# Optimization experiments

Measured on AMD Instinct MI355X. Metric: run time of the kernel, lower is better.

The kernel has to match this reference:

```python
import jax, jax.numpy as jnp
import numpy as np
from jax import lax

Q = 4          # decimation factor
N_ORDER = 8    # IIR filter order (scipy decimate default / explicit n=8)
RP = 0.05      # passband ripple in dB used by scipy.signal.decimate


def _cheby1_ba(N, rp, Wn):
    """Chebyshev type-I lowpass design, identical math to scipy.signal.cheby1."""
    eps = np.sqrt(10.0 ** (0.1 * rp) - 1.0)
    mu = np.arcsinh(1.0 / eps) / N
    k = np.arange(1, N + 1)
    theta = np.pi * (2 * k - 1) / (2 * N)
    # analog prototype poles (cheb1ap)
    p = -np.sinh(mu) * np.sin(theta) + 1j * np.cosh(mu) * np.cos(theta)
    g = np.prod(-p).real
    if N % 2 == 0:
        g /= np.sqrt(1.0 + eps ** 2)
    # frequency pre-warp (iirfilter with fs=2.0)
    fs = 2.0
    warped = 2.0 * fs * np.tan(np.pi * Wn / fs)
    # lp2lp_zpk
    p = p * warped
    g = g * warped ** N
    # bilinear_zpk
    fs2 = 2.0 * fs
    pd = (fs2 + p) / (fs2 - p)
    zd = -np.ones(N)  # N zeros at z=-1
    gd = g * np.real(1.0 / np.prod(fs2 - p))
    b = np.real(gd * np.poly(zd))
    a = np.real(np.poly(pd))
    return b, a


def _lfilter_zi(b, a):
    """Steady-state initial conditions, identical math to scipy.signal.lfilter_zi."""
    n = len(a)
    comp = np.zeros((n - 1, n - 1))
    comp[0, :] = -a[1:] / a[0]
    comp[1:, :-1] = np.eye(n - 2)
    IminusA = np.eye(n - 1) - comp.T
    B = b[1:] - a[1:] * b[0]
    return np.linalg.solve(IminusA, B)


_B_NP, _A_NP = _cheby1_ba(N_ORDER, RP, 0.8 / Q)
_ZI_NP = _lfilter_zi(_B_NP, _A_NP)


def _lfilter(b, a, x, zi):
    """IIR filter, direct-form II transposed. x: (T, M), zi: (order, M)."""
    def step(z, xt):
        yt = b[0] * xt + z[0]                       # (M,)
        z = jnp.concatenate([z[1:], jnp.zeros_like(z[:1])], axis=0) \
            + b[1:, None] * xt[None, :] - a[1:, None] * yt[None, :]
        return z, yt
    _, y = lax.scan(step, zi, x)
    return y


def _filtfilt(b, a, zi, x):
    """scipy.signal.filtfilt with padtype='odd', padlen=3*max(len(a),len(b)). x: (T, M)."""
    edge = 3 * b.shape[0]  # 27 for an order-8 filter
    left = 2.0 * x[0] - x[edge:0:-1]            # odd extension, left
    right = 2.0 * x[-1] - x[-2:-(edge + 2):-1]  # odd extension, right
    ext = jnp.concatenate([left, x, right], axis=0)
    y = _lfilter(b, a, ext, zi[:, None] * ext[0][None, :])          # forward pass
    y = _lfilter(b, a, y[::-1], zi[:, None] * y[-1][None, :])[::-1]  # backward pass
    return y[edge:-edge]


def _decimate(x):
    """scipy.signal.decimate(x, q=Q, n=8, ftype='iir', axis=-1, zero_phase=True)."""
    B_, C_, T = x.shape
    b = jnp.asarray(_B_NP, x.dtype)
    a = jnp.asarray(_A_NP, x.dtype)
    zi = jnp.asarray(_ZI_NP, x.dtype)
    xt = x.reshape(B_ * C_, T).T  # (T, M) -- time leading for lax.scan
    y = _filtfilt(b, a, zi, xt)
    y = y.T.reshape(B_, C_, T)
    return y[..., ::Q]


def setup_inputs() -> dict:
    key = jax.random.key(0)
    x = jax.random.normal(key, (32, 16, 65536), dtype=jnp.float32)
    return {"x": x}


def reference(x):
    return _decimate(x)
```

## Files before the change

kernel.cpp:

```cpp
#include <hip/hip_runtime.h>
#include <cmath>
#include <complex>

namespace {

constexpr int TLEN   = 65536;
constexpr int NCH    = 512;
constexpr size_t YB_ROWS = 16400;


struct Coefs {
  float b0,b1,b2,b3,b4,b5,b6,b7,b8;
  float na1,na2,na3,na4,na5,na6,na7,na8;
  float zi0,zi1,zi2,zi3,zi4,zi5,zi6,zi7;
};

#define IIR_STEP(xv, yv)                                  \
  do {                                                    \
    yv = fmaf(cf.b0, (xv), z0);                           \
    z0 = fmaf(cf.na1, yv, fmaf(cf.b1, (xv), z1));         \
    z1 = fmaf(cf.na2, yv, fmaf(cf.b2, (xv), z2));         \
    z2 = fmaf(cf.na3, yv, fmaf(cf.b3, (xv), z3));         \
    z3 = fmaf(cf.na4, yv, fmaf(cf.b4, (xv), z4));         \
    z4 = fmaf(cf.na5, yv, fmaf(cf.b5, (xv), z5));         \
    z5 = fmaf(cf.na6, yv, fmaf(cf.b6, (xv), z6));         \
    z6 = fmaf(cf.na7, yv, fmaf(cf.b7, (xv), z7));         \
    z7 = fmaf(cf.na8, yv, cf.b8 * (xv));                  \
  } while (0)

template<int QOFF, bool VEC>
__device__ __forceinline__ void run_chunk(const float* __restrict__ x,
                                          float* __restrict__ yb,
                                          const Coefs& cf,
                                          float (&lds)[2][4160],
                                          int m0, int e0, int nsub,
                                          int store_lo, int store_hi) {
  const int tid  = threadIdx.x;
  const int lane = tid & 63;
  const int vtbase = e0 - 27;
  const int mIdx = m0 + lane;
  float4* yq = reinterpret_cast<float4*>(yb);
  const int tq  = tid & 15;
  const int chb = tid >> 4;
  float4 rr0, rr1, rr2, rr3;
  float rs[16];

  auto issue = [&](int k) {
    const int vt0 = vtbase + 64 * k;
    if (VEC) {
      const float* p = x + (size_t)(m0 + chb) * TLEN + vt0 + 4 * tq;
      rr0 = *reinterpret_cast<const float4*>(p);
      rr1 = *reinterpret_cast<const float4*>(p + (size_t)16 * TLEN);
      rr2 = *reinterpret_cast<const float4*>(p + (size_t)32 * TLEN);
      rr3 = *reinterpret_cast<const float4*>(p + (size_t)48 * TLEN);
    } else {
#pragma unroll
      for (int i = 0; i < 16; ++i) {
        int idx = tid + 256 * i;
        int tl = idx & 63, ch = idx >> 6;
        int vt = vt0 + tl;
        const float* xr = x + (size_t)(m0 + ch) * TLEN;
        float v;
        if (vt < 0) v = 2.0f * xr[0] - xr[-vt];
        else if (vt >= TLEN) v = 2.0f * xr[TLEN - 1] - xr[2 * TLEN - 2 - vt];
        else v = xr[vt];
        rs[i] = v;
      }
    }
  };
  auto commit = [&](int k) {
    float* b = lds[k & 1];
    if (VEC) {
      const int base = 4 * tq * 65;
      b[base       + chb     ] = rr0.x; b[base + 65  + chb     ] = rr0.y;
      b[base + 130 + chb     ] = rr0.z; b[base + 195 + chb     ] = rr0.w;
      b[base       + chb + 16] = rr1.x; b[base + 65  + chb + 16] = rr1.y;
      b[base + 130 + chb + 16] = rr1.z; b[base + 195 + chb + 16] = rr1.w;
      b[base       + chb + 32] = rr2.x; b[base + 65  + chb + 32] = rr2.y;
      b[base + 130 + chb + 32] = rr2.z; b[base + 195 + chb + 32] = rr2.w;
      b[base       + chb + 48] = rr3.x; b[base + 65  + chb + 48] = rr3.y;
      b[base + 130 + chb + 48] = rr3.z; b[base + 195 + chb + 48] = rr3.w;
    } else {
#pragma unroll
      for (int i = 0; i < 16; ++i) {
        int idx = tid + 256 * i;
        int tl = idx & 63, ch = idx >> 6;
        b[tl * 65 + ch] = rs[i];
      }
    }
  };

  issue(0); commit(0);

  float z0 = 0, z1 = 0, z2 = 0, z3 = 0, z4 = 0, z5 = 0, z6 = 0, z7 = 0;
  float4 oq = make_float4(0.f, 0.f, 0.f, 0.f);

  for (int k = 0; k < nsub; ++k) {
    if (k + 1 < nsub) issue(k + 1);
    __syncthreads();
    if (k == 0 && tid < 64) {
      float x0 = lds[0][lane];
      z0 = cf.zi0 * x0; z1 = cf.zi1 * x0; z2 = cf.zi2 * x0; z3 = cf.zi3 * x0;
      z4 = cf.zi4 * x0; z5 = cf.zi5 * x0; z6 = cf.zi6 * x0; z7 = cf.zi7 * x0;
    }
    if (tid < 64) {
      const float* tile = lds[k & 1];
#pragma unroll
      for (int tl = 0; tl < 64; ++tl) {
        float xin = tile[tl * 65 + lane];
        float yv; IIR_STEP(xin, yv);
        if (QOFF == 1) {
          if (k == 0 && tl < 3) yb[2048 + mIdx * 4 + tl + 1] = yv;
        }
        const int q = (tl + QOFF) & 3;
        if (q == 0) oq.x = yv;
        else if (q == 1) oq.y = yv;
        else if (q == 2) oq.z = yv;
        else {
          oq.w = yv;
          const int step = 64 * k + tl;
          if (step >= store_lo && step <= store_hi)
            yq[(size_t)((e0 + step + 5) >> 2) * 512 + mIdx] = oq;
        }
      }
    }
    if (k + 1 < nsub) commit(k + 1);
  }
}

__global__ __launch_bounds__(256) void k_fwd2(const float* __restrict__ x,
                                              float* __restrict__ yb, Coefs cf) {
  __shared__ float lds[2][4160];
  const int c  = blockIdx.x;
  const int m0 = blockIdx.y * 64;
  if (c == 0)
    run_chunk<1, false>(x, yb, cf, lds, m0, 0, 8, 6, 510);
  else if (c == 128)
    run_chunk<0, false>(x, yb, cf, lds, m0, 65283, 5, 255, 307);
  else
    run_chunk<0, true>(x, yb, cf, lds, m0, 512 * c - 253, 12, 255, 763);
}

__global__ __launch_bounds__(256) void k_bwd2(const float* __restrict__ yb,
                                              float* __restrict__ out, Coefs cf) {
  __shared__ float wl[256 * 65];
  const int c   = blockIdx.x;
  const int tid = threadIdx.x;
  const int m   = blockIdx.y * 256 + tid;
  float z0, z1, z2, z3, z4, z5, z6, z7;
  int g_begin;
  if (c == 255) {
    float y0 = yb[(size_t)16398 * 2048 + (size_t)m * 4 + 2];
    z0 = cf.zi0 * y0; z1 = cf.zi1 * y0; z2 = cf.zi2 * y0; z3 = cf.zi3 * y0;
    z4 = cf.zi4 * y0; z5 = cf.zi5 * y0; z6 = cf.zi6 * y0; z7 = cf.zi7 * y0;
#pragma unroll
    for (int s = 65594; s >= 65584; --s) {
      float yin = yb[(size_t)(s >> 2) * 2048 + (size_t)m * 4 + (s & 3)];
      float wv; IIR_STEP(yin, wv);
      (void)wv;
    }
    g_begin = 16395;
  } else {
    g_begin = 64 * c + 139;
    float y0 = yb[(size_t)g_begin * 2048 + (size_t)m * 4 + 3];
    z0 = cf.zi0 * y0; z1 = cf.zi1 * y0; z2 = cf.zi2 * y0; z3 = cf.zi3 * y0;
    z4 = cf.zi4 * y0; z5 = cf.zi5 * y0; z6 = cf.zi6 * y0; z7 = cf.zi7 * y0;
  }
  const int g_stop = 64 * c + 11;
  const int g_hi   = 64 * c + 71;
  const float4* yv = reinterpret_cast<const float4*>(yb);
  auto ld = [&](int r) {
    int rr = r < 0 ? 0 : r;
    return yv[(size_t)rr * 512 + m];
  };
  float4 b0 = ld(g_begin), b1 = ld(g_begin - 1), b2 = ld(g_begin - 2), b3 = ld(g_begin - 3);
  float4 b4 = ld(g_begin - 4), b5 = ld(g_begin - 5), b6 = ld(g_begin - 6), b7 = ld(g_begin - 7);
  for (int g = g_begin; g >= g_stop; g -= 4) {
    float4 c0 = b0, c1 = b1, c2 = b2, c3 = b3;
    b0 = b4; b1 = b5; b2 = b6; b3 = b7;
    b4 = ld(g - 8); b5 = ld(g - 9); b6 = ld(g - 10); b7 = ld(g - 11);
    float4 pack;
#pragma unroll
    for (int j = 0; j < 4; ++j) {
      float4 q = (j == 0) ? c0 : (j == 1) ? c1 : (j == 2) ? c2 : c3;
      float w3, w2, w1, w0;
      IIR_STEP(q.w, w3);
      IIR_STEP(q.z, w2);
      IIR_STEP(q.y, w1);
      IIR_STEP(q.x, w0);
      (void)w3; (void)w2; (void)w1;
      if (j == 0) pack.w = w0;
      else if (j == 1) pack.z = w0;
      else if (j == 2) pack.y = w0;
      else pack.x = w0;
    }
    if (g <= g_hi) {
      const int cb = g - 11 - 64 * c;
      wl[tid * 65 + cb    ] = pack.x;
      wl[tid * 65 + cb + 1] = pack.y;
      wl[tid * 65 + cb + 2] = pack.z;
      wl[tid * 65 + cb + 3] = pack.w;
    }
  }
  __syncthreads();
  const int colb = 64 * c;
#pragma unroll
  for (int i = 0; i < 16; ++i) {
    int idx = tid + i * 256;
    int ch  = idx >> 4;
    int f4  = idx & 15;
    float4 v = make_float4(wl[ch * 65 + 4 * f4],     wl[ch * 65 + 4 * f4 + 1],
                           wl[ch * 65 + 4 * f4 + 2], wl[ch * 65 + 4 * f4 + 3]);
    *reinterpret_cast<float4*>(
        out + (size_t)(blockIdx.y * 256 + ch) * 16384 + colb + 4 * f4) = v;
  }
}

static void solve8(double Mm[8][9], double* zi) {
  for (int col = 0; col < 8; ++col) {
    int piv = col;
    for (int r = col + 1; r < 8; ++r)
      if (std::fabs(Mm[r][col]) > std::fabs(Mm[piv][col])) piv = r;
    if (piv != col)
      for (int j = 0; j < 9; ++j) { double t = Mm[col][j]; Mm[col][j] = Mm[piv][j]; Mm[piv][j] = t; }
    double d = Mm[col][col];
    for (int j = col; j < 9; ++j) Mm[col][j] /= d;
    for (int r = 0; r < 8; ++r)
      if (r != col) {
        double f = Mm[r][col];
        if (f != 0.0)
          for (int j = col; j < 9; ++j) Mm[r][j] -= f * Mm[col][j];
      }
  }
  for (int i = 0; i < 8; ++i) zi[i] = Mm[i][8];
}

static Coefs make_coefs() {
  using cd = std::complex<double>;
  const int N = 8;
  const double rp = 0.05, Wn = 0.8 / 4.0;
  double eps = std::sqrt(std::pow(10.0, 0.1 * rp) - 1.0);
  double mu = std::asinh(1.0 / eps) / N;
  cd p[8];
  for (int i = 0; i < N; ++i) {
    double th = M_PI * (2.0 * (i + 1) - 1.0) / (2.0 * N);
    p[i] = cd(-std::sinh(mu) * std::sin(th), std::cosh(mu) * std::cos(th));
  }
  cd pr(1.0, 0.0);
  for (int i = 0; i < N; ++i) pr *= -p[i];
  double g = pr.real();
  g /= std::sqrt(1.0 + eps * eps);
  const double fs = 2.0;
  double warped = 2.0 * fs * std::tan(M_PI * Wn / fs);
  for (int i = 0; i < N; ++i) p[i] *= warped;
  g *= std::pow(warped, (double)N);
  const double fs2 = 2.0 * fs;
  cd pd[8], dpr(1.0, 0.0);
  for (int i = 0; i < N; ++i) {
    pd[i] = (cd(fs2, 0.0) + p[i]) / (cd(fs2, 0.0) - p[i]);
    dpr *= (cd(fs2, 0.0) - p[i]);
  }
  double gd = g * (cd(1.0, 0.0) / dpr).real();
  static const double binom[9] = {1, 8, 28, 56, 70, 56, 28, 8, 1};
  double b[9], a[9];
  for (int i = 0; i < 9; ++i) b[i] = gd * binom[i];
  cd cp[9]; cp[0] = cd(1, 0);
  for (int i = 1; i < 9; ++i) cp[i] = cd(0, 0);
  for (int i = 0; i < N; ++i)
    for (int j = i + 1; j >= 1; --j) cp[j] -= pd[i] * cp[j - 1];
  for (int i = 0; i < 9; ++i) a[i] = cp[i].real();
  double Mm[8][9];
  for (int i = 0; i < 8; ++i) {
    for (int j = 0; j < 9; ++j) Mm[i][j] = 0.0;
    Mm[i][0] += a[i + 1];
    Mm[i][i] += 1.0;
    if (i < 7) Mm[i][i + 1] = -1.0;
    Mm[i][8] = b[i + 1] - a[i + 1] * b[0];
  }
  double zi[8];
  solve8(Mm, zi);
  Coefs cf;
  cf.b0 = (float)b[0]; cf.b1 = (float)b[1]; cf.b2 = (float)b[2]; cf.b3 = (float)b[3];
  cf.b4 = (float)b[4]; cf.b5 = (float)b[5]; cf.b6 = (float)b[6]; cf.b7 = (float)b[7];
  cf.b8 = (float)b[8];
  cf.na1 = (float)(-a[1]); cf.na2 = (float)(-a[2]); cf.na3 = (float)(-a[3]);
  cf.na4 = (float)(-a[4]); cf.na5 = (float)(-a[5]); cf.na6 = (float)(-a[6]);
  cf.na7 = (float)(-a[7]); cf.na8 = (float)(-a[8]);
  cf.zi0 = (float)zi[0]; cf.zi1 = (float)zi[1]; cf.zi2 = (float)zi[2]; cf.zi3 = (float)zi[3];
  cf.zi4 = (float)zi[4]; cf.zi5 = (float)zi[5]; cf.zi6 = (float)zi[6]; cf.zi7 = (float)zi[7];
  return cf;
}

}

extern "C" void kernel_launch(void* const* d_in, const int* in_sizes, int n_in,
                              void* d_out, int out_size, void* d_ws, size_t ws_size,
                              hipStream_t stream) {
  (void)in_sizes; (void)n_in; (void)out_size; (void)ws_size;
  const float* x = (const float*)d_in[0];
  float* out = (float*)d_out;
  float* yb  = (float*)d_ws;
  Coefs cf = make_coefs();
  hipLaunchKernelGGL(k_fwd2, dim3(129, NCH / 64), dim3(256), 0, stream, x, yb, cf);
  hipLaunchKernelGGL(k_bwd2, dim3(256, 2), dim3(256), 0, stream, yb, out, cf);
}
```

Baseline: 292.2 us.

## Double backward chunk length, merge tail chunk in forward, deepen prefetch

The backward kernel now handles 128 decimated outputs per block instead of 64, halving the grid to 128x2 blocks. This cuts the redundant warm-up recursion per output, since each chunk still spends a fixed lead-in. The forward kernel folds the former last tail block into the second-to-last block, using vector loads with a per-subchunk interior check. The backward loop prefetches three float4 rows ahead instead of two, and the LDS staging uses float4 stores. The trade-off is only 256 backward blocks of 256 threads, which lowers parallelism and latency hiding on a large GPU, plus more LDS per block.

```diff
diff --git a/kernel.cpp b/kernel.cpp
--- a/kernel.cpp
+++ b/kernel.cpp
@@ -45,9 +45,13 @@
   float4 rr0, rr1, rr2, rr3;
   float rs[16];
 
+  auto interior = [&](int k) {
+    const int vt0 = vtbase + 64 * k;
+    return vt0 >= 0 && vt0 + 63 < TLEN;
+  };
   auto issue = [&](int k) {
     const int vt0 = vtbase + 64 * k;
-    if (VEC) {
+    if (VEC && interior(k)) {
       const float* p = x + (size_t)(m0 + chb) * TLEN + vt0 + 4 * tq;
       rr0 = *reinterpret_cast<const float4*>(p);
       rr1 = *reinterpret_cast<const float4*>(p + (size_t)16 * TLEN);
@@ -70,7 +74,7 @@
   };
   auto commit = [&](int k) {
     float* b = lds[k & 1];
-    if (VEC) {
+    if (VEC && interior(k)) {
       const int base = 4 * tq * 65;
       b[base       + chb     ] = rr0.x; b[base + 65  + chb     ] = rr0.y;
       b[base + 130 + chb     ] = rr0.z; b[base + 195 + chb     ] = rr0.w;
@@ -135,21 +139,21 @@
   const int m0 = blockIdx.y * 64;
   if (c == 0)
     run_chunk<1, false>(x, yb, cf, lds, m0, 0, 8, 6, 510);
-  else if (c == 128)
-    run_chunk<0, false>(x, yb, cf, lds, m0, 65283, 5, 255, 307);
+  else if (c == 127)
+    run_chunk<0, true>(x, yb, cf, lds, m0, 512 * 127 - 253, 13, 255, 819);
   else
     run_chunk<0, true>(x, yb, cf, lds, m0, 512 * c - 253, 12, 255, 763);
 }
 
-__global__ __launch_bounds__(256) void k_bwd2(const float* __restrict__ yb,
+__global__ __launch_bounds__(256) void k_bwd3(const float* __restrict__ yb,
                                               float* __restrict__ out, Coefs cf) {
-  __shared__ float wl[256 * 65];
+  __shared__ float4 wl4[256 * 35];
   const int c   = blockIdx.x;
   const int tid = threadIdx.x;
   const int m   = blockIdx.y * 256 + tid;
   float z0, z1, z2, z3, z4, z5, z6, z7;
   int g_begin;
-  if (c == 255) {
+  if (c == 127) {
     float y0 = yb[(size_t)16398 * 2048 + (size_t)m * 4 + 2];
     z0 = cf.zi0 * y0; z1 = cf.zi1 * y0; z2 = cf.zi2 * y0; z3 = cf.zi3 * y0;
     z4 = cf.zi4 * y0; z5 = cf.zi5 * y0; z6 = cf.zi6 * y0; z7 = cf.zi7 * y0;
@@ -161,24 +165,26 @@
     }
     g_begin = 16395;
   } else {
-    g_begin = 64 * c + 139;
+    g_begin = 128 * c + 203;
     float y0 = yb[(size_t)g_begin * 2048 + (size_t)m * 4 + 3];
     z0 = cf.zi0 * y0; z1 = cf.zi1 * y0; z2 = cf.zi2 * y0; z3 = cf.zi3 * y0;
     z4 = cf.zi4 * y0; z5 = cf.zi5 * y0; z6 = cf.zi6 * y0; z7 = cf.zi7 * y0;
   }
-  const int g_stop = 64 * c + 11;
-  const int g_hi   = 64 * c + 71;
+  const int g_stop = 128 * c + 11;
+  const int g_hi   = 128 * c + 135;
   const float4* yv = reinterpret_cast<const float4*>(yb);
   auto ld = [&](int r) {
     int rr = r < 0 ? 0 : r;
     return yv[(size_t)rr * 512 + m];
   };
-  float4 b0 = ld(g_begin), b1 = ld(g_begin - 1), b2 = ld(g_begin - 2), b3 = ld(g_begin - 3);
-  float4 b4 = ld(g_begin - 4), b5 = ld(g_begin - 5), b6 = ld(g_begin - 6), b7 = ld(g_begin - 7);
+  float4 b0 = ld(g_begin),     b1 = ld(g_begin - 1),  b2 = ld(g_begin - 2),  b3 = ld(g_begin - 3);
+  float4 b4 = ld(g_begin - 4), b5 = ld(g_begin - 5),  b6 = ld(g_begin - 6),  b7 = ld(g_begin - 7);
+  float4 b8 = ld(g_begin - 8), b9 = ld(g_begin - 9), b10 = ld(g_begin - 10), b11 = ld(g_begin - 11);
   for (int g = g_begin; g >= g_stop; g -= 4) {
     float4 c0 = b0, c1 = b1, c2 = b2, c3 = b3;
-    b0 = b4; b1 = b5; b2 = b6; b3 = b7;
-    b4 = ld(g - 8); b5 = ld(g - 9); b6 = ld(g - 10); b7 = ld(g - 11);
+    b0 = b4; b1 = b5; b2 = b6;  b3 = b7;
+    b4 = b8; b5 = b9; b6 = b10; b7 = b11;
+    b8 = ld(g - 12); b9 = ld(g - 13); b10 = ld(g - 14); b11 = ld(g - 15);
     float4 pack;
 #pragma unroll
     for (int j = 0; j < 4; ++j) {
@@ -194,25 +200,17 @@
       else if (j == 2) pack.y = w0;
       else pack.x = w0;
     }
-    if (g <= g_hi) {
-      const int cb = g - 11 - 64 * c;
-      wl[tid * 65 + cb    ] = pack.x;
-      wl[tid * 65 + cb + 1] = pack.y;
-      wl[tid * 65 + cb + 2] = pack.z;
-      wl[tid * 65 + cb + 3] = pack.w;
-    }
+    if (g <= g_hi)
+      wl4[tid * 35 + (((g - 11) >> 2) - 32 * c)] = pack;
   }
   __syncthreads();
-  const int colb = 64 * c;
-#pragma unroll
-  for (int i = 0; i < 16; ++i) {
+  float4* outq = reinterpret_cast<float4*>(out);
+#pragma unroll
+  for (int i = 0; i < 32; ++i) {
     int idx = tid + i * 256;
-    int ch  = idx >> 4;
-    int f4  = idx & 15;
-    float4 v = make_float4(wl[ch * 65 + 4 * f4],     wl[ch * 65 + 4 * f4 + 1],
-                           wl[ch * 65 + 4 * f4 + 2], wl[ch * 65 + 4 * f4 + 3]);
-    *reinterpret_cast<float4*>(
-        out + (size_t)(blockIdx.y * 256 + ch) * 16384 + colb + 4 * f4) = v;
+    int ch  = idx >> 5;
+    int f4  = idx & 31;
+    outq[(size_t)(blockIdx.y * 256 + ch) * 4096 + 32 * c + f4] = wl4[ch * 35 + f4];
   }
 }
 
@@ -301,6 +299,6 @@
   float* out = (float*)d_out;
   float* yb  = (float*)d_ws;
   Coefs cf = make_coefs();
-  hipLaunchKernelGGL(k_fwd2, dim3(129, NCH / 64), dim3(256), 0, stream, x, yb, cf);
-  hipLaunchKernelGGL(k_bwd2, dim3(256, 2), dim3(256), 0, stream, yb, out, cf);
-}
+  hipLaunchKernelGGL(k_fwd2, dim3(128, NCH / 64), dim3(256), 0, stream, x, yb, cf);
+  hipLaunchKernelGGL(k_bwd3, dim3(128, 2), dim3(256), 0, stream, yb, out, cf);
+}
```

Result: slower. 306.5 us (+4.9%).
